# Performance work log

Hardware: AMD Instinct MI355X
Metric: run time of the kernel (lower is better)

## Reference

```python
import jax, jax.numpy as jnp
import numpy as np

FRAME, LATENT, HIDDEN, GATE_H, EXPERTS = 267, 32, 256, 64, 6
BATCH = 4096
IN0 = LATENT + FRAME            # 299: decoder layer-0 input (z, c)
IN1 = LATENT + HIDDEN           # 288: decoder layer-1/2 input (z, h)
OUT = FRAME                     # num_future_predictions * frame_size


def _lin(key, fan_in, fan_out):
    b = np.sqrt(1.0 / fan_in)
    return jax.random.uniform(key, (fan_in, fan_out), jnp.float32, -b, b)


def setup_inputs() -> dict:
    key = jax.random.key(0)
    ks = jax.random.split(key, 16)
    d = {
        "x": jax.random.normal(ks[0], (BATCH, FRAME), jnp.float32),
        "c": jax.random.normal(ks[1], (BATCH, FRAME), jnp.float32),
        "eps": jax.random.normal(ks[2], (BATCH, LATENT), jnp.float32),
        # encoder
        "enc_w1": _lin(ks[3], 2 * FRAME, HIDDEN), "enc_b1": jnp.zeros((HIDDEN,), jnp.float32),
        "enc_w2": _lin(ks[4], FRAME + HIDDEN, HIDDEN), "enc_b2": jnp.zeros((HIDDEN,), jnp.float32),
        "enc_wmu": _lin(ks[5], FRAME + HIDDEN, LATENT), "enc_bmu": jnp.zeros((LATENT,), jnp.float32),
        "enc_wlv": _lin(ks[6], FRAME + HIDDEN, LATENT), "enc_blv": jnp.zeros((LATENT,), jnp.float32),
        # gate MLP
        "g_w0": _lin(ks[7], IN0, GATE_H), "g_b0": jnp.zeros((GATE_H,), jnp.float32),
        "g_w1": _lin(ks[8], GATE_H, GATE_H), "g_b1": jnp.zeros((GATE_H,), jnp.float32),
        "g_w2": _lin(ks[9], GATE_H, EXPERTS), "g_b2": jnp.zeros((EXPERTS,), jnp.float32),
        # expert-mixed decoder layers (kaiming-uniform-ish init, bias 0.01)
        "w0": jax.random.uniform(ks[10], (EXPERTS, IN0, HIDDEN), jnp.float32, -np.sqrt(6.0 / IN0), np.sqrt(6.0 / IN0)),
        "b0": jnp.full((EXPERTS, HIDDEN), 0.01, jnp.float32),
        "w1": jax.random.uniform(ks[11], (EXPERTS, IN1, HIDDEN), jnp.float32, -np.sqrt(6.0 / IN1), np.sqrt(6.0 / IN1)),
        "b1": jnp.full((EXPERTS, HIDDEN), 0.01, jnp.float32),
        "w2": jax.random.uniform(ks[12], (EXPERTS, IN1, OUT), jnp.float32, -np.sqrt(6.0 / IN1), np.sqrt(6.0 / IN1)),
        "b2": jnp.full((EXPERTS, OUT), 0.01, jnp.float32),
    }
    return d


def reference(x, c, eps,
              enc_w1, enc_b1, enc_w2, enc_b2, enc_wmu, enc_bmu, enc_wlv, enc_blv,
              g_w0, g_b0, g_w1, g_b1, g_w2, g_b2,
              w0, b0, w1, b1, w2, b2):
    elu = jax.nn.elu
    # --- encoder ---
    h1 = elu(jnp.concatenate([x, c], axis=1) @ enc_w1 + enc_b1)
    h2 = elu(jnp.concatenate([x, h1], axis=1) @ enc_w2 + enc_b2)
    s = jnp.concatenate([x, h2], axis=1)
    mu = s @ enc_wmu + enc_bmu
    logvar = s @ enc_wlv + enc_blv
    z = mu + eps * jnp.exp(0.5 * logvar)
    # --- gate ---
    zc = jnp.concatenate([z, c], axis=1)
    g = elu(zc @ g_w0 + g_b0)
    g = elu(g @ g_w1 + g_b1)
    coeff = jax.nn.softmax(g @ g_w2 + g_b2, axis=1)  # [N, E]
    # --- soft-MoE decoder: blended-weight per-sample GEMMs ---
    layer = c
    for w, b, act in ((w0, b0, elu), (w1, b1, elu), (w2, b2, None)):
        inp = jnp.concatenate([z, layer], axis=1)  # [N, Din]
        # out[n,o] = sum_e coeff[n,e] * (inp[n,:] @ w[e,:,o]) + coeff[n,:] @ b[:,o]
        out = jnp.einsum('ne,ni,eio->no', coeff, inp, w) + coeff @ b
        layer = act(out) if act is not None else out
    return layer, mu, logvar
```

## Files before the change

### kernel.cpp

```cpp
#include <hip/hip_runtime.h>
#include <hip/hip_bf16.h>
#include <math.h>

#define N_BATCH 4096
#define FRAME   267
#define LATENT  32
#define HIDDEN  256
#define GATE_H  64
#define EXPERTS 6

typedef __hip_bfloat16 bf16;
typedef __bf16  bf16x8 __attribute__((ext_vector_type(8)));
typedef float   f32x4  __attribute__((ext_vector_type(4)));

__device__ __forceinline__ float eluf(float v) { return (v > 0.f) ? v : (expf(v) - 1.f); }

#define MFMA(a, b, p) __builtin_amdgcn_mfma_f32_16x16x32_bf16((a), (b), (p), 0, 0, 0)

struct WEnt { const float* src; bf16* dst; int K, M, Mtot, mOff, Ksteps, Mtiles, cum; };
struct WTab { WEnt e[10]; int total; };

__global__ __launch_bounds__(256) void prep_kernel(
    const float* __restrict__ bmu, const float* __restrict__ blv,
    float* __restrict__ biasCat, WTab tab)
{
    const int tid = threadIdx.x, bid = blockIdx.x;
    if (bid == 0 && tid < 64)
        biasCat[tid] = (tid < 32) ? bmu[tid] : blv[tid - 32];

    __shared__ float tbuf[32][33];
    int i = 0;
    while (i < 9 && bid >= tab.e[i + 1].cum) ++i;
    const WEnt en = tab.e[i];
    const int t = bid - en.cum;
    const int perE = en.Ksteps * en.Mtiles;
    const int e = t / perE;
    const int rr = t - e * perE;
    const int mt = rr / en.Ksteps;
    const int ks = rr - mt * en.Ksteps;
    const int tx = tid & 31, ty = tid >> 5;
    const float* src = en.src + (size_t)e * en.K * en.M;
    #pragma unroll
    for (int i0 = 0; i0 < 32; i0 += 8) {
        const int k = ks * 32 + i0 + ty, m = mt * 32 + tx;
        tbuf[i0 + ty][tx] = (k < en.K && m < en.M) ? src[(size_t)k * en.M + m] : 0.f;
    }
    __syncthreads();
    bf16* dst = en.dst + ((size_t)(e * en.Ksteps + ks) * en.Mtot + en.mOff + mt * 32) * 32;
    #pragma unroll
    for (int i0 = 0; i0 < 32; i0 += 8)
        dst[(size_t)(i0 + ty) * 32 + tx] = __float2bfloat16(tbuf[tx][i0 + ty]);
}

__global__ __launch_bounds__(512, 2) void fused_kernel(
    const float* __restrict__ x, const float* __restrict__ c,
    const float* __restrict__ eps,
    const bf16* __restrict__ We1, const float* __restrict__ eb1,
    const bf16* __restrict__ We2, const float* __restrict__ eb2,
    const bf16* __restrict__ Wml, const float* __restrict__ biasCat,
    const bf16* __restrict__ Wg0, const float* __restrict__ gb0,
    const bf16* __restrict__ Wg1, const float* __restrict__ gb1,
    const bf16* __restrict__ Wg2, const float* __restrict__ gb2,
    const bf16* __restrict__ W0, const float* __restrict__ b0,
    const bf16* __restrict__ W1, const float* __restrict__ b1,
    const bf16* __restrict__ W2, const float* __restrict__ b2,
    float* __restrict__ out_layer, float* __restrict__ out_mu,
    float* __restrict__ out_lv)
{
    __shared__ bf16  bufA[16 * 552];
    __shared__ bf16  bufB[16 * 552];
    __shared__ float sML[16 * 64];
    __shared__ bf16  sG1[16 * 72];
    __shared__ bf16  sG2[16 * 72];
    __shared__ float sLg[16 * 16];
    __shared__ float sCo[EXPERTS * 16];

    const int tid  = threadIdx.x;
    const int w    = tid >> 6, lane = tid & 63, ml = lane & 15, quad = lane >> 4;
    const int row0 = blockIdx.x * 16;
    const int r32  = tid >> 5, l32 = tid & 31;

    {
        const float* xr = x + (size_t)(row0 + r32) * FRAME;
        const float* cr = c + (size_t)(row0 + r32) * FRAME;
        #pragma unroll
        for (int j = 0; j < 17; ++j) {
            const int col = l32 + j * 32;
            float v = 0.f;
            if (col < FRAME)          v = xr[col];
            else if (col < 2 * FRAME) v = cr[col - FRAME];
            bufA[r32 * 552 + col] = __float2bfloat16(v);
        }
    }
    __syncthreads();

    {
        bf16x8 av[17];
        #pragma unroll
        for (int ks = 0; ks < 17; ++ks)
            av[ks] = *(const bf16x8*)(bufA + ml * 552 + ks * 32 + quad * 8);
        const int col0 = 32 * w + ml;
        f32x4 p0 = (f32x4){0,0,0,0}, p1 = (f32x4){0,0,0,0};
        const bf16* wp = We1 + (size_t)col0 * 32 + quad * 8;
        #pragma unroll
        for (int ks = 0; ks < 17; ++ks) {
            p0 = MFMA(av[ks], *(const bf16x8*)(wp + (size_t)ks * 256 * 32), p0);
            p1 = MFMA(av[ks], *(const bf16x8*)(wp + (size_t)ks * 256 * 32 + 16 * 32), p1);
        }
        const float bv0 = eb1[col0], bv1 = eb1[col0 + 16];
        #pragma unroll
        for (int rg = 0; rg < 4; ++rg) {
            bufB[(quad * 4 + rg) * 552 + 267 + col0]      = __float2bfloat16(eluf(p0[rg] + bv0));
            bufB[(quad * 4 + rg) * 552 + 267 + col0 + 16] = __float2bfloat16(eluf(p1[rg] + bv1));
        }
        #pragma unroll
        for (int j = 0; j < 9; ++j) {
            const int cc = l32 + j * 32;
            if (cc < 267) bufB[r32 * 552 + cc] = bufA[r32 * 552 + cc];
            else          bufB[r32 * 552 + (cc - 267 + 523)] = __float2bfloat16(0.f);
        }
    }
    __syncthreads();

    {
        bf16x8 av[17];
        #pragma unroll
        for (int ks = 0; ks < 17; ++ks)
            av[ks] = *(const bf16x8*)(bufB + ml * 552 + ks * 32 + quad * 8);
        const int col0 = 32 * w + ml;
        f32x4 p0 = (f32x4){0,0,0,0}, p1 = (f32x4){0,0,0,0};
        const bf16* wp = We2 + (size_t)col0 * 32 + quad * 8;
        #pragma unroll
        for (int ks = 0; ks < 17; ++ks) {
            p0 = MFMA(av[ks], *(const bf16x8*)(wp + (size_t)ks * 256 * 32), p0);
            p1 = MFMA(av[ks], *(const bf16x8*)(wp + (size_t)ks * 256 * 32 + 16 * 32), p1);
        }
        __syncthreads();
        const float bv0 = eb2[col0], bv1 = eb2[col0 + 16];
        #pragma unroll
        for (int rg = 0; rg < 4; ++rg) {
            bufB[(quad * 4 + rg) * 552 + 267 + col0]      = __float2bfloat16(eluf(p0[rg] + bv0));
            bufB[(quad * 4 + rg) * 552 + 267 + col0 + 16] = __float2bfloat16(eluf(p1[rg] + bv1));
        }
    }
    __syncthreads();

    if (w < 4) {
        const int col = 16 * w + ml;
        f32x4 p = (f32x4){0,0,0,0};
        const bf16* wp = Wml + (size_t)col * 32 + quad * 8;
        #pragma unroll
        for (int ks = 0; ks < 17; ++ks) {
            const bf16x8 av = *(const bf16x8*)(bufB + ml * 552 + ks * 32 + quad * 8);
            p = MFMA(av, *(const bf16x8*)(wp + (size_t)ks * 64 * 32), p);
        }
        const float bv = biasCat[col];
        #pragma unroll
        for (int rg = 0; rg < 4; ++rg)
            sML[(quad * 4 + rg) * 64 + col] = p[rg] + bv;
    }
    __syncthreads();

    {
        const float m  = sML[r32 * 64 + l32];
        const float lv = sML[r32 * 64 + 32 + l32];
        const int gi = (row0 + r32) * LATENT + l32;
        out_mu[gi] = m; out_lv[gi] = lv;
        const bf16 zb = __float2bfloat16(m + eps[gi] * expf(0.5f * lv));
        bufA[r32 * 552 + l32] = zb;
        bufB[r32 * 552 + l32] = zb;
        #pragma unroll
        for (int j = 0; j < 9; ++j) {
            const int col = 32 + l32 + j * 32;
            bf16 v = __float2bfloat16(0.f);
            if (col < 299) v = bufA[r32 * 552 + 267 + (col - 32)];
            bufB[r32 * 552 + col] = v;
        }
    }
    __syncthreads();

    if (w < 4) {
        const int col = 16 * w + ml;
        f32x4 p = (f32x4){0,0,0,0};
        const bf16* wp = Wg0 + (size_t)col * 32 + quad * 8;
        #pragma unroll
        for (int ks = 0; ks < 10; ++ks)
            p = MFMA(*(const bf16x8*)(bufB + ml * 552 + ks * 32 + quad * 8),
                     *(const bf16x8*)(wp + (size_t)ks * 64 * 32), p);
        const float bv = gb0[col];
        #pragma unroll
        for (int rg = 0; rg < 4; ++rg)
            sG1[(quad * 4 + rg) * 72 + col] = __float2bfloat16(eluf(p[rg] + bv));
    }
    __syncthreads();

    if (w < 4) {
        const int col = 16 * w + ml;
        f32x4 p = (f32x4){0,0,0,0};
        const bf16* wp = Wg1 + (size_t)col * 32 + quad * 8;
        #pragma unroll
        for (int ks = 0; ks < 2; ++ks)
            p = MFMA(*(const bf16x8*)(sG1 + ml * 72 + ks * 32 + quad * 8),
                     *(const bf16x8*)(wp + (size_t)ks * 64 * 32), p);
        const float bv = gb1[col];
        #pragma unroll
        for (int rg = 0; rg < 4; ++rg)
            sG2[(quad * 4 + rg) * 72 + col] = __float2bfloat16(eluf(p[rg] + bv));
    }
    __syncthreads();

    if (w == 0) {
        f32x4 p = (f32x4){0,0,0,0};
        const bf16* wp = Wg2 + (size_t)ml * 32 + quad * 8;
        #pragma unroll
        for (int ks = 0; ks < 2; ++ks)
            p = MFMA(*(const bf16x8*)(sG2 + ml * 72 + ks * 32 + quad * 8),
                     *(const bf16x8*)(wp + (size_t)ks * 32 * 32), p);
        const float bv = (ml < EXPERTS) ? gb2[ml] : 0.f;
        #pragma unroll
        for (int rg = 0; rg < 4; ++rg)
            sLg[(quad * 4 + rg) * 16 + ml] = p[rg] + bv;
    }
    __syncthreads();

    if (tid < 16) {
        float v[EXPERTS];
        float m = -1e30f;
        #pragma unroll
        for (int i = 0; i < EXPERTS; ++i) { v[i] = sLg[tid * 16 + i]; m = fmaxf(m, v[i]); }
        float s = 0.f;
        #pragma unroll
        for (int i = 0; i < EXPERTS; ++i) { v[i] = expf(v[i] - m); s += v[i]; }
        const float inv = 1.f / s;
        #pragma unroll
        for (int i = 0; i < EXPERTS; ++i) sCo[i * 16 + tid] = v[i] * inv;
    }
    __syncthreads();

    {
        bf16x8 av[10];
        #pragma unroll
        for (int ks = 0; ks < 10; ++ks)
            av[ks] = *(const bf16x8*)(bufB + ml * 552 + ks * 32 + quad * 8);
        const int col0 = 32 * w + ml;
        f32x4 acc0 = (f32x4){0,0,0,0}, acc1 = (f32x4){0,0,0,0};
        for (int e = 0; e < EXPERTS; ++e) {
            f32x4 p0 = (f32x4){0,0,0,0}, p1 = (f32x4){0,0,0,0};
            const bf16* wp = W0 + ((size_t)e * 10 * 256 + col0) * 32 + quad * 8;
            #pragma unroll
            for (int ks = 0; ks < 10; ++ks) {
                p0 = MFMA(av[ks], *(const bf16x8*)(wp + (size_t)ks * 256 * 32), p0);
                p1 = MFMA(av[ks], *(const bf16x8*)(wp + (size_t)ks * 256 * 32 + 16 * 32), p1);
            }
            const float bv0 = b0[e * 256 + col0], bv1 = b0[e * 256 + col0 + 16];
            #pragma unroll
            for (int rg = 0; rg < 4; ++rg) {
                const float cf = sCo[e * 16 + quad * 4 + rg];
                acc0[rg] += cf * (p0[rg] + bv0);
                acc1[rg] += cf * (p1[rg] + bv1);
            }
        }
        #pragma unroll
        for (int rg = 0; rg < 4; ++rg) {
            bufA[(quad * 4 + rg) * 552 + 32 + col0]      = __float2bfloat16(eluf(acc0[rg]));
            bufA[(quad * 4 + rg) * 552 + 32 + col0 + 16] = __float2bfloat16(eluf(acc1[rg]));
        }
    }
    __syncthreads();

    {
        bf16x8 av[9];
        #pragma unroll
        for (int ks = 0; ks < 9; ++ks)
            av[ks] = *(const bf16x8*)(bufA + ml * 552 + ks * 32 + quad * 8);
        const int col0 = 32 * w + ml;
        f32x4 acc0 = (f32x4){0,0,0,0}, acc1 = (f32x4){0,0,0,0};
        for (int e = 0; e < EXPERTS; ++e) {
            f32x4 p0 = (f32x4){0,0,0,0}, p1 = (f32x4){0,0,0,0};
            const bf16* wp = W1 + ((size_t)e * 9 * 256 + col0) * 32 + quad * 8;
            #pragma unroll
            for (int ks = 0; ks < 9; ++ks) {
                p0 = MFMA(av[ks], *(const bf16x8*)(wp + (size_t)ks * 256 * 32), p0);
                p1 = MFMA(av[ks], *(const bf16x8*)(wp + (size_t)ks * 256 * 32 + 16 * 32), p1);
            }
            const float bv0 = b1[e * 256 + col0], bv1 = b1[e * 256 + col0 + 16];
            #pragma unroll
            for (int rg = 0; rg < 4; ++rg) {
                const float cf = sCo[e * 16 + quad * 4 + rg];
                acc0[rg] += cf * (p0[rg] + bv0);
                acc1[rg] += cf * (p1[rg] + bv1);
            }
        }
        __syncthreads();
        #pragma unroll
        for (int rg = 0; rg < 4; ++rg) {
            bufB[(quad * 4 + rg) * 552 + 32 + col0]      = __float2bfloat16(eluf(acc0[rg]));
            bufB[(quad * 4 + rg) * 552 + 32 + col0 + 16] = __float2bfloat16(eluf(acc1[rg]));
        }
    }
    __syncthreads();

    {
        bf16x8 av[9];
        #pragma unroll
        for (int ks = 0; ks < 9; ++ks)
            av[ks] = *(const bf16x8*)(bufB + ml * 552 + ks * 32 + quad * 8);
        for (int t = w; t < 18; t += 8) {
            const int col = 16 * t + ml;
            f32x4 acc = (f32x4){0,0,0,0};
            for (int e = 0; e < EXPERTS; ++e) {
                f32x4 p = (f32x4){0,0,0,0};
                const bf16* wp = W2 + ((size_t)e * 9 * 320 + col) * 32 + quad * 8;
                #pragma unroll
                for (int ks = 0; ks < 9; ++ks)
                    p = MFMA(av[ks], *(const bf16x8*)(wp + (size_t)ks * 320 * 32), p);
                const float bv = (col < FRAME) ? b2[e * FRAME + col] : 0.f;
                #pragma unroll
                for (int rg = 0; rg < 4; ++rg)
                    acc[rg] += sCo[e * 16 + quad * 4 + rg] * (p[rg] + bv);
            }
            if (col < FRAME) {
                #pragma unroll
                for (int rg = 0; rg < 4; ++rg)
                    out_layer[(size_t)(row0 + quad * 4 + rg) * FRAME + col] = acc[rg];
            }
        }
    }
}

extern "C" void kernel_launch(void* const* d_in, const int* in_sizes, int n_in,
                              void* d_out, int out_size, void* d_ws, size_t ws_size,
                              hipStream_t stream) {
    const float* x       = (const float*)d_in[0];
    const float* c       = (const float*)d_in[1];
    const float* eps     = (const float*)d_in[2];
    const float* enc_w1  = (const float*)d_in[3];
    const float* enc_b1  = (const float*)d_in[4];
    const float* enc_w2  = (const float*)d_in[5];
    const float* enc_b2  = (const float*)d_in[6];
    const float* enc_wmu = (const float*)d_in[7];
    const float* enc_bmu = (const float*)d_in[8];
    const float* enc_wlv = (const float*)d_in[9];
    const float* enc_blv = (const float*)d_in[10];
    const float* g_w0    = (const float*)d_in[11];
    const float* g_b0    = (const float*)d_in[12];
    const float* g_w1    = (const float*)d_in[13];
    const float* g_b1    = (const float*)d_in[14];
    const float* g_w2    = (const float*)d_in[15];
    const float* g_b2    = (const float*)d_in[16];
    const float* w0      = (const float*)d_in[17];
    const float* b0      = (const float*)d_in[18];
    const float* w1      = (const float*)d_in[19];
    const float* b1      = (const float*)d_in[20];
    const float* w2      = (const float*)d_in[21];
    const float* b2      = (const float*)d_in[22];

    float* out_layer = (float*)d_out;
    float* out_mu    = out_layer + (size_t)N_BATCH * FRAME;
    float* out_lv    = out_mu    + (size_t)N_BATCH * LATENT;

    char* p = (char*)d_ws;
    float* biasCat = (float*)p;  p += 64 * 4;
    bf16* Wt_e1 = (bf16*)p;      p += (size_t)17 * 256 * 32 * 2;
    bf16* Wt_e2 = (bf16*)p;      p += (size_t)17 * 256 * 32 * 2;
    bf16* Wt_ml = (bf16*)p;      p += (size_t)17 * 64 * 32 * 2;
    bf16* Wt_g0 = (bf16*)p;      p += (size_t)10 * 64 * 32 * 2;
    bf16* Wt_g1 = (bf16*)p;      p += (size_t)2 * 64 * 32 * 2;
    bf16* Wt_g2 = (bf16*)p;      p += (size_t)2 * 32 * 32 * 2;
    bf16* Wt_w0 = (bf16*)p;      p += (size_t)EXPERTS * 10 * 256 * 32 * 2;
    bf16* Wt_w1 = (bf16*)p;      p += (size_t)EXPERTS * 9 * 256 * 32 * 2;
    bf16* Wt_w2 = (bf16*)p;      p += (size_t)EXPERTS * 9 * 320 * 32 * 2;

    WTab tab;
    int cum = 0, n = 0;
    auto add = [&](const float* src, bf16* dst, int K, int M, int Mtot, int mOff, int E) {
        int Ksteps;
        if (K == 534 || K == 523) Ksteps = 17;
        else if (K == 299) Ksteps = 10;
        else if (K == 288) Ksteps = 9;
        else Ksteps = 2;
        const int Mtiles = (M + 31) / 32;
        tab.e[n] = {src, dst, K, M, Mtot, mOff, Ksteps, Mtiles, cum};
        cum += E * Ksteps * Mtiles;
        ++n;
    };
    add(enc_w1,  Wt_e1, 534, 256, 256, 0, 1);
    add(enc_w2,  Wt_e2, 523, 256, 256, 0, 1);
    add(enc_wmu, Wt_ml, 523, 32, 64, 0, 1);
    add(enc_wlv, Wt_ml, 523, 32, 64, 32, 1);
    add(g_w0,    Wt_g0, 299, 64, 64, 0, 1);
    add(g_w1,    Wt_g1, 64, 64, 64, 0, 1);
    add(g_w2,    Wt_g2, 64, 6, 32, 0, 1);
    add(w0,      Wt_w0, 299, 256, 256, 0, EXPERTS);
    add(w1,      Wt_w1, 288, 256, 256, 0, EXPERTS);
    add(w2,      Wt_w2, 288, 267, 320, 0, EXPERTS);
    tab.total = cum;

    prep_kernel<<<dim3(cum), dim3(256), 0, stream>>>(enc_bmu, enc_blv, biasCat, tab);

    fused_kernel<<<dim3(N_BATCH / 16), dim3(512), 0, stream>>>(
        x, c, eps,
        Wt_e1, enc_b1, Wt_e2, enc_b2, Wt_ml, biasCat,
        Wt_g0, g_b0, Wt_g1, g_b1, Wt_g2, g_b2,
        Wt_w0, b0, Wt_w1, b1, Wt_w2, b2,
        out_layer, out_mu, out_lv);
}
```

Baseline: 187.5 us.

## Raise occupancy target and restructure fused kernel loads, split mu/logvar K work

Raises the launch bound to four blocks per CU and drops the per-layer A-fragment register arrays, re-reading activations from shared memory inside the MFMA loops so register pressure fits the higher occupancy. The mu/logvar projection is split across all eight waves by K halves, with partial sums reduced through a doubled shared buffer. Input staging is reorganised to wave-per-row loads, the expert loops are fully unrolled, one barrier in the decoder layer-1 epilogue is removed, and the output layer skips a padding-only column tile. The gains rely on more resident waves hiding latency, at the cost of more LDS reads and possible register spilling under the tighter bound.

```diff
diff --git a/kernel.cpp b/kernel.cpp
--- a/kernel.cpp
+++ b/kernel.cpp
@@ -52,7 +52,7 @@
         dst[(size_t)(i0 + ty) * 32 + tx] = __float2bfloat16(tbuf[tx][i0 + ty]);
 }
 
-__global__ __launch_bounds__(512, 2) void fused_kernel(
+__global__ __launch_bounds__(512, 4) void fused_kernel(
     const float* __restrict__ x, const float* __restrict__ c,
     const float* __restrict__ eps,
     const bf16* __restrict__ We1, const float* __restrict__ eb1,
@@ -69,7 +69,7 @@
 {
     __shared__ bf16  bufA[16 * 552];
     __shared__ bf16  bufB[16 * 552];
-    __shared__ float sML[16 * 64];
+    __shared__ float sMLp[2][16 * 64];
     __shared__ bf16  sG1[16 * 72];
     __shared__ bf16  sG2[16 * 72];
     __shared__ float sLg[16 * 16];
@@ -78,151 +78,153 @@
     const int tid  = threadIdx.x;
     const int w    = tid >> 6, lane = tid & 63, ml = lane & 15, quad = lane >> 4;
     const int row0 = blockIdx.x * 16;
-    const int r32  = tid >> 5, l32 = tid & 31;
-
-    {
-        const float* xr = x + (size_t)(row0 + r32) * FRAME;
-        const float* cr = c + (size_t)(row0 + r32) * FRAME;
-        #pragma unroll
-        for (int j = 0; j < 17; ++j) {
-            const int col = l32 + j * 32;
-            float v = 0.f;
-            if (col < FRAME)          v = xr[col];
-            else if (col < 2 * FRAME) v = cr[col - FRAME];
-            bufA[r32 * 552 + col] = __float2bfloat16(v);
-        }
-    }
-    __syncthreads();
-
-    {
-        bf16x8 av[17];
-        #pragma unroll
-        for (int ks = 0; ks < 17; ++ks)
-            av[ks] = *(const bf16x8*)(bufA + ml * 552 + ks * 32 + quad * 8);
+
+    {
+        #pragma unroll
+        for (int rr = 0; rr < 2; ++rr) {
+            const int r = w + rr * 8;
+            const float* xr = x + (size_t)(row0 + r) * FRAME;
+            const float* cr = c + (size_t)(row0 + r) * FRAME;
+            #pragma unroll
+            for (int j = 0; j < 9; ++j) {
+                const int col = lane + j * 64;
+                if (col < 544) {
+                    float v = 0.f;
+                    if (col < FRAME)          v = xr[col];
+                    else if (col < 2 * FRAME) v = cr[col - FRAME];
+                    bufA[r * 552 + col] = __float2bfloat16(v);
+                }
+            }
+        }
+    }
+    __syncthreads();
+
+    {
         const int col0 = 32 * w + ml;
-        f32x4 p0 = (f32x4){0,0,0,0}, p1 = (f32x4){0,0,0,0};
-        const bf16* wp = We1 + (size_t)col0 * 32 + quad * 8;
+        const bf16* wq0 = We1 + (size_t)col0 * 32 + quad * 8;
+        const bf16* wq1 = wq0 + 16 * 32;
+        f32x4 a0 = (f32x4){0,0,0,0}, a1 = (f32x4){0,0,0,0};
         #pragma unroll
         for (int ks = 0; ks < 17; ++ks) {
-            p0 = MFMA(av[ks], *(const bf16x8*)(wp + (size_t)ks * 256 * 32), p0);
-            p1 = MFMA(av[ks], *(const bf16x8*)(wp + (size_t)ks * 256 * 32 + 16 * 32), p1);
+            const bf16x8 a = *(const bf16x8*)(bufA + ml * 552 + ks * 32 + quad * 8);
+            a0 = MFMA(a, *(const bf16x8*)(wq0 + (size_t)ks * 8192), a0);
+            a1 = MFMA(a, *(const bf16x8*)(wq1 + (size_t)ks * 8192), a1);
         }
         const float bv0 = eb1[col0], bv1 = eb1[col0 + 16];
         #pragma unroll
         for (int rg = 0; rg < 4; ++rg) {
-            bufB[(quad * 4 + rg) * 552 + 267 + col0]      = __float2bfloat16(eluf(p0[rg] + bv0));
-            bufB[(quad * 4 + rg) * 552 + 267 + col0 + 16] = __float2bfloat16(eluf(p1[rg] + bv1));
-        }
-        #pragma unroll
-        for (int j = 0; j < 9; ++j) {
-            const int cc = l32 + j * 32;
-            if (cc < 267) bufB[r32 * 552 + cc] = bufA[r32 * 552 + cc];
-            else          bufB[r32 * 552 + (cc - 267 + 523)] = __float2bfloat16(0.f);
-        }
-    }
-    __syncthreads();
-
-    {
-        bf16x8 av[17];
-        #pragma unroll
-        for (int ks = 0; ks < 17; ++ks)
-            av[ks] = *(const bf16x8*)(bufB + ml * 552 + ks * 32 + quad * 8);
+            bufB[(quad * 4 + rg) * 552 + 267 + col0]      = __float2bfloat16(eluf(a0[rg] + bv0));
+            bufB[(quad * 4 + rg) * 552 + 267 + col0 + 16] = __float2bfloat16(eluf(a1[rg] + bv1));
+        }
+        #pragma unroll
+        for (int rr = 0; rr < 2; ++rr) {
+            const int r = w + rr * 8;
+            #pragma unroll
+            for (int j = 0; j < 5; ++j) {
+                const int cc = lane + j * 64;
+                if (cc < 267) bufB[r * 552 + cc] = bufA[r * 552 + cc];
+            }
+            if (lane < 21) bufB[r * 552 + 523 + lane] = __float2bfloat16(0.f);
+        }
+    }
+    __syncthreads();
+
+    {
         const int col0 = 32 * w + ml;
-        f32x4 p0 = (f32x4){0,0,0,0}, p1 = (f32x4){0,0,0,0};
-        const bf16* wp = We2 + (size_t)col0 * 32 + quad * 8;
+        const bf16* wq0 = We2 + (size_t)col0 * 32 + quad * 8;
+        const bf16* wq1 = wq0 + 16 * 32;
+        f32x4 a0 = (f32x4){0,0,0,0}, a1 = (f32x4){0,0,0,0};
         #pragma unroll
         for (int ks = 0; ks < 17; ++ks) {
-            p0 = MFMA(av[ks], *(const bf16x8*)(wp + (size_t)ks * 256 * 32), p0);
-            p1 = MFMA(av[ks], *(const bf16x8*)(wp + (size_t)ks * 256 * 32 + 16 * 32), p1);
+            const bf16x8 a = *(const bf16x8*)(bufB + ml * 552 + ks * 32 + quad * 8);
+            a0 = MFMA(a, *(const bf16x8*)(wq0 + (size_t)ks * 8192), a0);
+            a1 = MFMA(a, *(const bf16x8*)(wq1 + (size_t)ks * 8192), a1);
         }
         __syncthreads();
         const float bv0 = eb2[col0], bv1 = eb2[col0 + 16];
         #pragma unroll
         for (int rg = 0; rg < 4; ++rg) {
-            bufB[(quad * 4 + rg) * 552 + 267 + col0]      = __float2bfloat16(eluf(p0[rg] + bv0));
-            bufB[(quad * 4 + rg) * 552 + 267 + col0 + 16] = __float2bfloat16(eluf(p1[rg] + bv1));
+            bufB[(quad * 4 + rg) * 552 + 267 + col0]      = __float2bfloat16(eluf(a0[rg] + bv0));
+            bufB[(quad * 4 + rg) * 552 + 267 + col0 + 16] = __float2bfloat16(eluf(a1[rg] + bv1));
+        }
+    }
+    __syncthreads();
+
+    {
+        const int ct = w & 3, kg = w >> 2;
+        const int col = 16 * ct + ml;
+        const int k0 = kg ? 9 : 0, k1 = kg ? 17 : 9;
+        const bf16* wq = Wml + (size_t)col * 32 + quad * 8;
+        f32x4 p = (f32x4){0,0,0,0};
+        for (int ks = k0; ks < k1; ++ks)
+            p = MFMA(*(const bf16x8*)(bufB + ml * 552 + ks * 32 + quad * 8),
+                     *(const bf16x8*)(wq + (size_t)ks * 2048), p);
+        #pragma unroll
+        for (int rg = 0; rg < 4; ++rg)
+            sMLp[kg][(quad * 4 + rg) * 64 + col] = p[rg];
+    }
+    __syncthreads();
+
+    {
+        const int r = tid >> 5, l = tid & 31;
+        const float m  = sMLp[0][r * 64 + l] + sMLp[1][r * 64 + l] + biasCat[l];
+        const float lv = sMLp[0][r * 64 + 32 + l] + sMLp[1][r * 64 + 32 + l] + biasCat[32 + l];
+        const int gi = (row0 + r) * LATENT + l;
+        out_mu[gi] = m; out_lv[gi] = lv;
+        const bf16 zb = __float2bfloat16(m + eps[gi] * expf(0.5f * lv));
+        bufA[r * 552 + l] = zb;
+        bufB[r * 552 + l] = zb;
+        #pragma unroll
+        for (int j = 0; j < 9; ++j) {
+            const int col = 32 + l + j * 32;
+            bf16 v = __float2bfloat16(0.f);
+            if (col < 299) v = bufA[r * 552 + 267 + (col - 32)];
+            bufB[r * 552 + col] = v;
         }
     }
     __syncthreads();
 
     if (w < 4) {
         const int col = 16 * w + ml;
+        const bf16* gq = Wg0 + (size_t)col * 32 + quad * 8;
         f32x4 p = (f32x4){0,0,0,0};
-        const bf16* wp = Wml + (size_t)col * 32 + quad * 8;
-        #pragma unroll
-        for (int ks = 0; ks < 17; ++ks) {
-            const bf16x8 av = *(const bf16x8*)(bufB + ml * 552 + ks * 32 + quad * 8);
-            p = MFMA(av, *(const bf16x8*)(wp + (size_t)ks * 64 * 32), p);
-        }
-        const float bv = biasCat[col];
+        #pragma unroll
+        for (int ks = 0; ks < 10; ++ks)
+            p = MFMA(*(const bf16x8*)(bufB + ml * 552 + ks * 32 + quad * 8),
+                     *(const bf16x8*)(gq + (size_t)ks * 2048), p);
+        const float bv = gb0[col];
         #pragma unroll
         for (int rg = 0; rg < 4; ++rg)
-            sML[(quad * 4 + rg) * 64 + col] = p[rg] + bv;
-    }
-    __syncthreads();
-
-    {
-        const float m  = sML[r32 * 64 + l32];
-        const float lv = sML[r32 * 64 + 32 + l32];
-        const int gi = (row0 + r32) * LATENT + l32;
-        out_mu[gi] = m; out_lv[gi] = lv;
-        const bf16 zb = __float2bfloat16(m + eps[gi] * expf(0.5f * lv));
-        bufA[r32 * 552 + l32] = zb;
-        bufB[r32 * 552 + l32] = zb;
-        #pragma unroll
-        for (int j = 0; j < 9; ++j) {
-            const int col = 32 + l32 + j * 32;
-            bf16 v = __float2bfloat16(0.f);
-            if (col < 299) v = bufA[r32 * 552 + 267 + (col - 32)];
-            bufB[r32 * 552 + col] = v;
-        }
-    }
-    __syncthreads();
-
+            sG1[(quad * 4 + rg) * 72 + col] = __float2bfloat16(eluf(p[rg] + bv));
+    }
+    __syncthreads();
     if (w < 4) {
         const int col = 16 * w + ml;
+        const bf16* gq = Wg1 + (size_t)col * 32 + quad * 8;
         f32x4 p = (f32x4){0,0,0,0};
-        const bf16* wp = Wg0 + (size_t)col * 32 + quad * 8;
-        #pragma unroll
-        for (int ks = 0; ks < 10; ++ks)
-            p = MFMA(*(const bf16x8*)(bufB + ml * 552 + ks * 32 + quad * 8),
-                     *(const bf16x8*)(wp + (size_t)ks * 64 * 32), p);
-        const float bv = gb0[col];
-        #pragma unroll
-        for (int rg = 0; rg < 4; ++rg)
-            sG1[(quad * 4 + rg) * 72 + col] = __float2bfloat16(eluf(p[rg] + bv));
-    }
-    __syncthreads();
-
-    if (w < 4) {
-        const int col = 16 * w + ml;
-        f32x4 p = (f32x4){0,0,0,0};
-        const bf16* wp = Wg1 + (size_t)col * 32 + quad * 8;
         #pragma unroll
         for (int ks = 0; ks < 2; ++ks)
             p = MFMA(*(const bf16x8*)(sG1 + ml * 72 + ks * 32 + quad * 8),
-                     *(const bf16x8*)(wp + (size_t)ks * 64 * 32), p);
+                     *(const bf16x8*)(gq + (size_t)ks * 2048), p);
         const float bv = gb1[col];
         #pragma unroll
         for (int rg = 0; rg < 4; ++rg)
             sG2[(quad * 4 + rg) * 72 + col] = __float2bfloat16(eluf(p[rg] + bv));
     }
     __syncthreads();
-
     if (w == 0) {
+        const bf16* gq = Wg2 + (size_t)ml * 32 + quad * 8;
         f32x4 p = (f32x4){0,0,0,0};
-        const bf16* wp = Wg2 + (size_t)ml * 32 + quad * 8;
         #pragma unroll
         for (int ks = 0; ks < 2; ++ks)
             p = MFMA(*(const bf16x8*)(sG2 + ml * 72 + ks * 32 + quad * 8),
-                     *(const bf16x8*)(wp + (size_t)ks * 32 * 32), p);
+                     *(const bf16x8*)(gq + (size_t)ks * 1024), p);
         const float bv = (ml < EXPERTS) ? gb2[ml] : 0.f;
         #pragma unroll
         for (int rg = 0; rg < 4; ++rg)
             sLg[(quad * 4 + rg) * 16 + ml] = p[rg] + bv;
     }
     __syncthreads();
-
     if (tid < 16) {
         float v[EXPERTS];
         float m = -1e30f;
@@ -238,19 +240,18 @@
     __syncthreads();
 
     {
-        bf16x8 av[10];
-        #pragma unroll
-        for (int ks = 0; ks < 10; ++ks)
-            av[ks] = *(const bf16x8*)(bufB + ml * 552 + ks * 32 + quad * 8);
         const int col0 = 32 * w + ml;
+        const bf16* wq0 = W0 + (size_t)col0 * 32 + quad * 8;
+        const bf16* wq1 = wq0 + 16 * 32;
         f32x4 acc0 = (f32x4){0,0,0,0}, acc1 = (f32x4){0,0,0,0};
+        #pragma unroll
         for (int e = 0; e < EXPERTS; ++e) {
             f32x4 p0 = (f32x4){0,0,0,0}, p1 = (f32x4){0,0,0,0};
-            const bf16* wp = W0 + ((size_t)e * 10 * 256 + col0) * 32 + quad * 8;
             #pragma unroll
             for (int ks = 0; ks < 10; ++ks) {
-                p0 = MFMA(av[ks], *(const bf16x8*)(wp + (size_t)ks * 256 * 32), p0);
-                p1 = MFMA(av[ks], *(const bf16x8*)(wp + (size_t)ks * 256 * 32 + 16 * 32), p1);
+                const bf16x8 a = *(const bf16x8*)(bufB + ml * 552 + ks * 32 + quad * 8);
+                p0 = MFMA(a, *(const bf16x8*)(wq0 + (size_t)(e * 10 + ks) * 8192), p0);
+                p1 = MFMA(a, *(const bf16x8*)(wq1 + (size_t)(e * 10 + ks) * 8192), p1);
             }
             const float bv0 = b0[e * 256 + col0], bv1 = b0[e * 256 + col0 + 16];
             #pragma unroll
@@ -269,19 +270,18 @@
     __syncthreads();
 
     {
-        bf16x8 av[9];
-        #pragma unroll
-        for (int ks = 0; ks < 9; ++ks)
-            av[ks] = *(const bf16x8*)(bufA + ml * 552 + ks * 32 + quad * 8);
         const int col0 = 32 * w + ml;
+        const bf16* wq0 = W1 + (size_t)col0 * 32 + quad * 8;
+        const bf16* wq1 = wq0 + 16 * 32;
         f32x4 acc0 = (f32x4){0,0,0,0}, acc1 = (f32x4){0,0,0,0};
+        #pragma unroll
         for (int e = 0; e < EXPERTS; ++e) {
             f32x4 p0 = (f32x4){0,0,0,0}, p1 = (f32x4){0,0,0,0};
-            const bf16* wp = W1 + ((size_t)e * 9 * 256 + col0) * 32 + quad * 8;
             #pragma unroll
             for (int ks = 0; ks < 9; ++ks) {
-                p0 = MFMA(av[ks], *(const bf16x8*)(wp + (size_t)ks * 256 * 32), p0);
-                p1 = MFMA(av[ks], *(const bf16x8*)(wp + (size_t)ks * 256 * 32 + 16 * 32), p1);
+                const bf16x8 a = *(const bf16x8*)(bufA + ml * 552 + ks * 32 + quad * 8);
+                p0 = MFMA(a, *(const bf16x8*)(wq0 + (size_t)(e * 9 + ks) * 8192), p0);
+                p1 = MFMA(a, *(const bf16x8*)(wq1 + (size_t)(e * 9 + ks) * 8192), p1);
             }
             const float bv0 = b1[e * 256 + col0], bv1 = b1[e * 256 + col0 + 16];
             #pragma unroll
@@ -291,7 +291,6 @@
                 acc1[rg] += cf * (p1[rg] + bv1);
             }
         }
-        __syncthreads();
         #pragma unroll
         for (int rg = 0; rg < 4; ++rg) {
             bufB[(quad * 4 + rg) * 552 + 32 + col0]      = __float2bfloat16(eluf(acc0[rg]));
@@ -301,19 +300,17 @@
     __syncthreads();
 
     {
-        bf16x8 av[9];
-        #pragma unroll
-        for (int ks = 0; ks < 9; ++ks)
-            av[ks] = *(const bf16x8*)(bufB + ml * 552 + ks * 32 + quad * 8);
-        for (int t = w; t < 18; t += 8) {
+        for (int t = w; t < 17; t += 8) {
             const int col = 16 * t + ml;
+            const bf16* wq = W2 + (size_t)col * 32 + quad * 8;
             f32x4 acc = (f32x4){0,0,0,0};
+            #pragma unroll
             for (int e = 0; e < EXPERTS; ++e) {
                 f32x4 p = (f32x4){0,0,0,0};
-                const bf16* wp = W2 + ((size_t)e * 9 * 320 + col) * 32 + quad * 8;
                 #pragma unroll
                 for (int ks = 0; ks < 9; ++ks)
-                    p = MFMA(av[ks], *(const bf16x8*)(wp + (size_t)ks * 320 * 32), p);
+                    p = MFMA(*(const bf16x8*)(bufB + ml * 552 + ks * 32 + quad * 8),
+                             *(const bf16x8*)(wq + (size_t)(e * 9 + ks) * 10240), p);
                 const float bv = (col < FRAME) ? b2[e * FRAME + col] : 0.f;
                 #pragma unroll
                 for (int rg = 0; rg < 4; ++rg)
```

After: 182.8 us. 2.5% less time.
